# Performance work log

Hardware: AMD Instinct MI355X
Metric: run time of the kernel (lower is better)

Reference implementation:

```python
import jax, jax.numpy as jnp
import numpy as np

GROUP_SIZE = 128
ZERO_POINT = 8  # symmetric int4 zero point


def setup_inputs() -> dict:
    key = jax.random.key(0)
    k1, k2, k3 = jax.random.split(key, 3)
    M, K, N = 8192, 4096, 4096
    x = jax.random.normal(k1, (M, K), dtype=jnp.float16)
    # logical unpacked int4 codes in [0, 16)
    q_weight = jax.random.randint(k2, (K, N), 0, 16, dtype=jnp.int32)
    # per-group scales, small positive values like real quantized checkpoints
    scale = (jax.random.uniform(k3, (K // GROUP_SIZE, N), dtype=jnp.float32) * 0.02 + 0.001).astype(jnp.float16)
    return {"x": x, "q_weight": q_weight, "scale": scale}


def reference(x, q_weight, scale):
    # Dequantize: w[k, n] = (q[k, n] - zp) * scale[k // group, n]
    K, N = q_weight.shape
    g = K // scale.shape[0]  # group size
    scale_full = jnp.repeat(scale, g, axis=0)  # [K, N]
    w = (q_weight.astype(jnp.float16) - jnp.float16(ZERO_POINT)) * scale_full
    # GEMM with fp32 accumulation, fp16 output (Marlin semantics)
    y = jnp.dot(x, w, preferred_element_type=jnp.float32).astype(jnp.float16)
    return y
```

## Files before the change

kernel.cpp:

```cpp
#include <hip/hip_runtime.h>
#include <stdint.h>
#include <math.h>

#define GROUP 128
#define ZP 8
#define BM 256
#define BN 256
#define BK 32

typedef short short8 __attribute__((ext_vector_type(8)));
typedef float floatx4 __attribute__((ext_vector_type(4)));

typedef __attribute__((address_space(3))) void lds_void;
typedef const __attribute__((address_space(1))) void gbl_void;
#define GLOAD_LDS16(g, l) \
  __builtin_amdgcn_global_load_lds((gbl_void*)(g), (lds_void*)(l), 16, 0, 0)

#define VMCNT(n) asm volatile("s_waitcnt vmcnt(" #n ")" ::: "memory")
#define LGKM0()  asm volatile("s_waitcnt lgkmcnt(0)" ::: "memory")
#define BAR()    __builtin_amdgcn_s_barrier()
#define SCHEDB() __builtin_amdgcn_sched_barrier(0)

__device__ __forceinline__ ushort f2bf(float f) {
    union { float f; uint32_t i; } v; v.f = f;
    uint32_t r = v.i + 0x7FFF + ((v.i >> 16) & 1);
    return (ushort)(r >> 16);
}

__global__ __launch_bounds__(256) void conv_x_kernel(
    const float* __restrict__ x, ushort* __restrict__ xb, size_t total8)
{
    const size_t stride = (size_t)gridDim.x * 256;
    for (size_t id = (size_t)blockIdx.x * 256 + threadIdx.x; id < total8; id += stride) {
        const float4 a = *reinterpret_cast<const float4*>(x + id * 8);
        const float4 b = *reinterpret_cast<const float4*>(x + id * 8 + 4);
        ushort o[8] __attribute__((aligned(16)));
        o[0] = f2bf(a.x); o[1] = f2bf(a.y); o[2] = f2bf(a.z); o[3] = f2bf(a.w);
        o[4] = f2bf(b.x); o[5] = f2bf(b.y); o[6] = f2bf(b.z); o[7] = f2bf(b.w);
        *reinterpret_cast<uint4*>(xb + id * 8) = *reinterpret_cast<const uint4*>(o);
    }
}

__global__ __launch_bounds__(256) void dequant_t_kernel(
    const int* __restrict__ q, const float* __restrict__ scale,
    ushort* __restrict__ wt, int K, int N)
{
    __shared__ ushort T[64 * 68];
    const int t  = threadIdx.x;
    const int k0 = blockIdx.x * 64;
    const int n0 = blockIdx.y * 64;
    const int g  = k0 / GROUP;
    const int c  = (t & 15) * 4;
    const int r0 = (t >> 4);

    const float4 s = *reinterpret_cast<const float4*>(&scale[(size_t)g * N + n0 + c]);

#pragma unroll
    for (int j = 0; j < 4; ++j) {
        const int r = r0 + j * 16;
        const int4 qv = *reinterpret_cast<const int4*>(&q[(size_t)(k0 + r) * N + n0 + c]);
        T[(c + 0) * 68 + r] = f2bf((float)(qv.x - ZP) * s.x);
        T[(c + 1) * 68 + r] = f2bf((float)(qv.y - ZP) * s.y);
        T[(c + 2) * 68 + r] = f2bf((float)(qv.z - ZP) * s.z);
        T[(c + 3) * 68 + r] = f2bf((float)(qv.w - ZP) * s.w);
    }
    __syncthreads();
#pragma unroll
    for (int j = 0; j < 4; ++j) {
        const int nn = r0 + j * 16;
        const int kk = c;
        const uint2 v = *reinterpret_cast<const uint2*>(&T[nn * 68 + kk]);
        *reinterpret_cast<uint2*>(&wt[(size_t)(n0 + nn) * K + k0 + kk]) = v;
    }
}

__global__ __launch_bounds__(512, 2) void gemm256_ring_kernel(
    const ushort* __restrict__ Ab, const ushort* __restrict__ Wt,
    float* __restrict__ out, int M, int N, int K)
{
    __shared__ ushort smem[4 * 16384];

    const int bid = blockIdx.x;
    const int nwg = gridDim.x;
    int wg = bid;
    if ((nwg & 7) == 0) {
        const int cpx = nwg >> 3;
        wg = (bid & 7) * cpx + (bid >> 3);
    }
    const int ntn = N / BN;
    const int m0 = (wg / ntn) * BM;
    const int n0 = (wg % ntn) * BN;

    const int t    = threadIdx.x;
    const int lane = t & 63;
    const int w    = t >> 6;
    const int wm   = w >> 2;
    const int wn   = w & 3;
    const int NT   = K / BK;

    const ushort* pa[2]; const ushort* pb[2];
    int dstA[2], dstB[2];
#pragma unroll
    for (int s = 0; s < 2; ++s) {
        const int r = s * 128 + (t >> 2);
        const int j = (t & 3) ^ ((r >> 1) & 3);
        pa[s] = Ab + (size_t)(m0 + r) * K + j * 8;
        pb[s] = Wt + (size_t)(n0 + r) * K + j * 8;
        dstA[s] = s * 8192 + t * 16;
        dstB[s] = 16384 + s * 8192 + t * 16;
    }

    int aoff[8], boff[4];
#pragma unroll
    for (int i = 0; i < 8; ++i) {
        const int r = wm * 128 + i * 16 + (lane & 15);
        aoff[i] = r * 64 + (((lane >> 4) ^ ((r >> 1) & 3)) << 4);
    }
#pragma unroll
    for (int j = 0; j < 4; ++j) {
        const int r = wn * 64 + j * 16 + (lane & 15);
        boff[j] = 16384 + r * 64 + (((lane >> 4) ^ ((r >> 1) & 3)) << 4);
    }

    floatx4 acc[8][4];
#pragma unroll
    for (int i = 0; i < 8; ++i)
#pragma unroll
        for (int j = 0; j < 4; ++j) acc[i][j] = floatx4{0.f, 0.f, 0.f, 0.f};

#pragma unroll
    for (int U = 0; U < 3; ++U) {
        char* sb = (char*)smem + U * 32768;
        GLOAD_LDS16(pa[0] + U * 32, sb + dstA[0]);
        GLOAD_LDS16(pa[1] + U * 32, sb + dstA[1]);
        GLOAD_LDS16(pb[0] + U * 32, sb + dstB[0]);
        GLOAD_LDS16(pb[1] + U * 32, sb + dstB[1]);
    }
    VMCNT(8);
    BAR();

    auto body = [&](int T, bool issue) __attribute__((always_inline)) {
        if (issue) {
            char* sb = (char*)smem + ((T + 3) & 3) * 32768;
            const int ko = (T + 3) * 32;
            GLOAD_LDS16(pa[0] + ko, sb + dstA[0]);
            GLOAD_LDS16(pa[1] + ko, sb + dstA[1]);
            GLOAD_LDS16(pb[0] + ko, sb + dstB[0]);
            GLOAD_LDS16(pb[1] + ko, sb + dstB[1]);
        }
        const char* sb = (const char*)smem + (T & 3) * 32768;
        short8 af[8], bf[4];
#pragma unroll
        for (int i = 0; i < 8; ++i)
            af[i] = *reinterpret_cast<const short8*>(sb + aoff[i]);
#pragma unroll
        for (int j = 0; j < 4; ++j)
            bf[j] = *reinterpret_cast<const short8*>(sb + boff[j]);
        __builtin_amdgcn_s_setprio(1);
#pragma unroll
        for (int i = 0; i < 8; ++i)
#pragma unroll
            for (int j = 0; j < 4; ++j)
                acc[i][j] = __builtin_amdgcn_mfma_f32_16x16x32_bf16(af[i], bf[j], acc[i][j], 0, 0, 0);
        __builtin_amdgcn_s_setprio(0);
        LGKM0();
        SCHEDB();
    };

    for (int T = 0; T + 3 < NT; ++T) {
        body(T, true);
        VMCNT(8);
        BAR();
    }
    body(NT - 3, false); VMCNT(4); BAR();
    body(NT - 2, false); VMCNT(0); BAR();
    body(NT - 1, false);

    const int orow0 = m0 + wm * 128 + (lane >> 4) * 4;
    const int ocol0 = n0 + wn * 64 + (lane & 15);
#pragma unroll
    for (int i = 0; i < 8; ++i)
#pragma unroll
        for (int j = 0; j < 4; ++j)
#pragma unroll
            for (int r = 0; r < 4; ++r)
                out[(size_t)(orow0 + i * 16 + r) * N + ocol0 + j * 16] = acc[i][j][r];
}

#define MR 16
__global__ __launch_bounds__(256) void naive_kernel(
    const float* __restrict__ x, const int* __restrict__ q,
    const float* __restrict__ sc, float* __restrict__ out,
    int M, int N, int K)
{
    const int n  = blockIdx.x * 256 + threadIdx.x;
    const int m0 = blockIdx.y * MR;
    float acc[MR];
#pragma unroll
    for (int i = 0; i < MR; ++i) acc[i] = 0.f;
    for (int k = 0; k < K; ++k) {
        const float s = sc[(size_t)(k / GROUP) * N + n];
        const float w = (float)(q[(size_t)k * N + n] - ZP) * s;
#pragma unroll
        for (int i = 0; i < MR; ++i)
            acc[i] = fmaf(x[(size_t)(m0 + i) * K + k], w, acc[i]);
    }
#pragma unroll
    for (int i = 0; i < MR; ++i)
        out[(size_t)(m0 + i) * N + n] = acc[i];
}

extern "C" void kernel_launch(void* const* d_in, const int* in_sizes, int n_in,
                              void* d_out, int out_size, void* d_ws, size_t ws_size,
                              hipStream_t stream) {
    const float* x  = (const float*)d_in[0];
    const int*   q  = (const int*)d_in[1];
    const float* sc = (const float*)d_in[2];
    float*       o  = (float*)d_out;

    int M = 8192, K = 4096, N = 4096;
    if (!((long long)in_sizes[0] == (long long)M * K &&
          (long long)in_sizes[1] == (long long)K * N &&
          (long long)out_size    == (long long)M * N)) {
        const double S0 = (double)in_sizes[0], S1 = (double)in_sizes[1];
        K = (int)llround(sqrt(S0 * S1 / (double)out_size));
        N = in_sizes[1] / K;
        M = in_sizes[0] / K;
    }

    const size_t xb_bytes = (size_t)M * K * 2;
    const size_t wt_bytes = (size_t)N * K * 2;

    const bool ok = (M % BM == 0) && (N % BN == 0) && (K % BK == 0) &&
                    (K / BK >= 4) && (N % 64 == 0) && (K % 64 == 0) &&
                    (K % GROUP == 0) && (ws_size >= xb_bytes + wt_bytes);

    if (ok) {
        ushort* xb = (ushort*)d_ws;
        ushort* wt = (ushort*)((char*)d_ws + xb_bytes);
        conv_x_kernel<<<2048, 256, 0, stream>>>(x, xb, (size_t)M * K / 8);
        dequant_t_kernel<<<dim3(K / 64, N / 64), 256, 0, stream>>>(q, sc, wt, K, N);
        const int ngemm = (M / BM) * (N / BN);
        gemm256_ring_kernel<<<dim3(ngemm), 512, 0, stream>>>(xb, wt, o, M, N, K);
    } else {
        naive_kernel<<<dim3(N / 256, M / MR), 256, 0, stream>>>(x, q, sc, o, M, N, K);
    }
}
```

Baseline: 294.8 us.

## Split GEMM K-step into two half-windows interleaving LDS reads, loads and MFMAs

Each K-iteration of the main GEMM loop becomes two phases. Each phase reads half of the A fragments, issues half of the global-to-LDS prefetch loads, then runs 16 MFMAs, and extra workgroup barriers separate the phases. The aim is to spread LDS reads and global loads across the MFMA work, so the waves' memory traffic is staggered against matrix compute and register pressure from the fragments drops. The cost is three extra barriers per iteration, which can stall waves and hurt throughput.

```diff
diff --git a/kernel.cpp b/kernel.cpp
--- a/kernel.cpp
+++ b/kernel.cpp
@@ -139,42 +139,55 @@
     VMCNT(8);
     BAR();
 
-    auto body = [&](int T, bool issue) __attribute__((always_inline)) {
-        if (issue) {
-            char* sb = (char*)smem + ((T + 3) & 3) * 32768;
-            const int ko = (T + 3) * 32;
-            GLOAD_LDS16(pa[0] + ko, sb + dstA[0]);
-            GLOAD_LDS16(pa[1] + ko, sb + dstA[1]);
-            GLOAD_LDS16(pb[0] + ko, sb + dstB[0]);
-            GLOAD_LDS16(pb[1] + ko, sb + dstB[1]);
-        }
+    auto window = [&](int T, bool issue) __attribute__((always_inline)) {
         const char* sb = (const char*)smem + (T & 3) * 32768;
+        char* sd = (char*)smem + ((T + 3) & 3) * 32768;
+        const int ko = (T + 3) * 32;
         short8 af[8], bf[4];
 #pragma unroll
-        for (int i = 0; i < 8; ++i)
+        for (int i = 0; i < 4; ++i)
             af[i] = *reinterpret_cast<const short8*>(sb + aoff[i]);
 #pragma unroll
         for (int j = 0; j < 4; ++j)
             bf[j] = *reinterpret_cast<const short8*>(sb + boff[j]);
+        if (issue) {
+            GLOAD_LDS16(pa[0] + ko, sd + dstA[0]);
+            GLOAD_LDS16(pa[1] + ko, sd + dstA[1]);
+        }
+        BAR(); LGKM0(); SCHEDB();
         __builtin_amdgcn_s_setprio(1);
 #pragma unroll
-        for (int i = 0; i < 8; ++i)
+        for (int i = 0; i < 4; ++i)
 #pragma unroll
             for (int j = 0; j < 4; ++j)
                 acc[i][j] = __builtin_amdgcn_mfma_f32_16x16x32_bf16(af[i], bf[j], acc[i][j], 0, 0, 0);
         __builtin_amdgcn_s_setprio(0);
-        LGKM0();
-        SCHEDB();
+        BAR();
+#pragma unroll
+        for (int i = 4; i < 8; ++i)
+            af[i] = *reinterpret_cast<const short8*>(sb + aoff[i]);
+        if (issue) {
+            GLOAD_LDS16(pb[0] + ko, sd + dstB[0]);
+            GLOAD_LDS16(pb[1] + ko, sd + dstB[1]);
+        }
+        BAR(); LGKM0(); SCHEDB();
+        __builtin_amdgcn_s_setprio(1);
+#pragma unroll
+        for (int i = 4; i < 8; ++i)
+#pragma unroll
+            for (int j = 0; j < 4; ++j)
+                acc[i][j] = __builtin_amdgcn_mfma_f32_16x16x32_bf16(af[i], bf[j], acc[i][j], 0, 0, 0);
+        __builtin_amdgcn_s_setprio(0);
     };
 
     for (int T = 0; T + 3 < NT; ++T) {
-        body(T, true);
+        window(T, true);
         VMCNT(8);
         BAR();
     }
-    body(NT - 3, false); VMCNT(4); BAR();
-    body(NT - 2, false); VMCNT(0); BAR();
-    body(NT - 1, false);
+    window(NT - 3, false); VMCNT(4); BAR();
+    window(NT - 2, false); VMCNT(0); BAR();
+    window(NT - 1, false);
 
     const int orow0 = m0 + wm * 128 + (lane >> 4) * 4;
     const int ocol0 = n0 + wn * 64 + (lane & 15);
```

Measured after the change: 300.1 us. No clear change (+1.8%).

## Restructure GEMM LDS ring into paired-stage double buffering with one barrier per two tiles

Applied to the files above, without the earlier changes.

The K-loop goes from a 4-slot ring that prefetches 3 tiles ahead and synchronises after every 32-wide tile to a scheme that loads two K-tiles at a time into the other half of the buffer. It then computes two tiles and waits with vmcnt(0) plus one barrier per pair. This halves the number of barriers and waitcnt points per K step. In exchange the prefetch distance shrinks and each iteration waits for all outstanding loads, so memory latency may be less well hidden.

```diff
diff --git a/kernel.cpp b/kernel.cpp
--- a/kernel.cpp
+++ b/kernel.cpp
@@ -129,25 +129,29 @@
         for (int j = 0; j < 4; ++j) acc[i][j] = floatx4{0.f, 0.f, 0.f, 0.f};
 
 #pragma unroll
-    for (int U = 0; U < 3; ++U) {
+    for (int U = 0; U < 2; ++U) {
         char* sb = (char*)smem + U * 32768;
         GLOAD_LDS16(pa[0] + U * 32, sb + dstA[0]);
         GLOAD_LDS16(pa[1] + U * 32, sb + dstA[1]);
         GLOAD_LDS16(pb[0] + U * 32, sb + dstB[0]);
         GLOAD_LDS16(pb[1] + U * 32, sb + dstB[1]);
     }
-    VMCNT(8);
+    VMCNT(0);
     BAR();
 
-    auto body = [&](int T, bool issue) __attribute__((always_inline)) {
-        if (issue) {
-            char* sb = (char*)smem + ((T + 3) & 3) * 32768;
-            const int ko = (T + 3) * 32;
-            GLOAD_LDS16(pa[0] + ko, sb + dstA[0]);
-            GLOAD_LDS16(pa[1] + ko, sb + dstA[1]);
-            GLOAD_LDS16(pb[0] + ko, sb + dstB[0]);
-            GLOAD_LDS16(pb[1] + ko, sb + dstB[1]);
+    auto stagepair = [&](int T2) __attribute__((always_inline)) {
+#pragma unroll
+        for (int U = 0; U < 2; ++U) {
+            char* sd = (char*)smem + ((T2 + U) & 3) * 32768;
+            const int ko = (T2 + U) * 32;
+            GLOAD_LDS16(pa[0] + ko, sd + dstA[0]);
+            GLOAD_LDS16(pa[1] + ko, sd + dstA[1]);
+            GLOAD_LDS16(pb[0] + ko, sd + dstB[0]);
+            GLOAD_LDS16(pb[1] + ko, sd + dstB[1]);
         }
+    };
+
+    auto sub = [&](int T) __attribute__((always_inline)) {
         const char* sb = (const char*)smem + (T & 3) * 32768;
         short8 af[8], bf[4];
 #pragma unroll
@@ -163,18 +167,20 @@
             for (int j = 0; j < 4; ++j)
                 acc[i][j] = __builtin_amdgcn_mfma_f32_16x16x32_bf16(af[i], bf[j], acc[i][j], 0, 0, 0);
         __builtin_amdgcn_s_setprio(0);
+    };
+
+    const int NW = NT / 2;
+    for (int W = 0; W < NW - 1; ++W) {
+        stagepair(2 * W + 2);
+        sub(2 * W);
+        sub(2 * W + 1);
         LGKM0();
         SCHEDB();
-    };
-
-    for (int T = 0; T + 3 < NT; ++T) {
-        body(T, true);
-        VMCNT(8);
+        VMCNT(0);
         BAR();
     }
-    body(NT - 3, false); VMCNT(4); BAR();
-    body(NT - 2, false); VMCNT(0); BAR();
-    body(NT - 1, false);
+    sub(2 * NW - 2);
+    sub(2 * NW - 1);
 
     const int orow0 = m0 + wm * 128 + (lane >> 4) * 4;
     const int ocol0 = n0 + wn * 64 + (lane & 15);
@@ -231,8 +237,8 @@
     const size_t xb_bytes = (size_t)M * K * 2;
     const size_t wt_bytes = (size_t)N * K * 2;
 
-    const bool ok = (M % BM == 0) && (N % BN == 0) && (K % BK == 0) &&
-                    (K / BK >= 4) && (N % 64 == 0) && (K % 64 == 0) &&
+    const bool ok = (M % BM == 0) && (N % BN == 0) && (K % 64 == 0) &&
+                    (K / BK >= 4) && (N % 64 == 0) &&
                     (K % GROUP == 0) && (ws_size >= xb_bytes + wt_bytes);
 
     if (ok) {
```

New measurement: 301.8 us. 1.02x slower.
